# Performance work log

Hardware: AMD Instinct MI355X
Metric: run time of the kernel (lower is better)

Reference implementation:

```python
import jax, jax.numpy as jnp
import numpy as np

G_NUMS = 30      # group_nums
G_SIZE = 100     # group_size (also neighborhood_size)
BETA = 1.0
EPS = 1e-9


def setup_inputs() -> dict:
    key = jax.random.key(0)
    pointclouds = jax.random.normal(key, (8, 131072, 3), dtype=jnp.float32)
    return {"pointclouds": pointclouds}


def _knn_gather(points, queries, k):
    """points [b,N,3], queries [b,G,3] -> k nearest points per query [b,G,k,3]."""
    # squared distances [b,G,N]
    d2 = (
        jnp.sum(queries * queries, axis=-1)[..., None]
        - 2.0 * jnp.einsum("bgd,bnd->bgn", queries, points)
        + jnp.sum(points * points, axis=-1)[:, None, :]
    )
    _, idx = jax.lax.top_k(-d2, k)                    # [b,G,k]
    nbrs = jax.vmap(lambda p, i: p[i])(points, idx)   # [b,G,k,3]
    return nbrs


def reference(pointclouds):
    b, N, _ = pointclouds.shape
    # --- group_points: uniform-stride sampled centers, k-NN groups, group means ---
    stride = N // G_NUMS
    centers = pointclouds[:, ::stride][:, :G_NUMS]                 # [b,G,3]
    grouped = _knn_gather(pointclouds, centers, G_SIZE)            # [b,G,K,3]
    group_means = jnp.mean(grouped, axis=2)                        # [b,G,3]

    # --- estimate_pointcloud_local_coord_frames: per-group 3x3 PCA ---
    nbrs = _knn_gather(pointclouds, group_means, G_SIZE)           # [b,G,K,3]
    mu = jnp.mean(nbrs, axis=2, keepdims=True)
    X = nbrs - mu
    cov = jnp.einsum("bgkd,bgke->bgde", X, X) / G_SIZE             # [b,G,3,3]
    curvatures, frames = jnp.linalg.eigh(cov)                      # eigvals ascending

    # --- elongated-shape loss ---
    denom = curvatures[..., 0] + curvatures[..., 1] + curvatures[..., 2] + EPS
    first_vec = curvatures[..., 2] / denom
    second_vec = curvatures[..., 1] / denom
    elongated_shape_loss = -jnp.sum(first_vec - second_vec) / b

    # --- angular smoothness cost over group means / principal directions ---
    dirs = frames[..., :, 2]                                       # [b,G,3] largest-eig direction
    dm = jnp.sum(
        (group_means[:, :, None, :] - group_means[:, None, :, :]) ** 2, axis=-1
    )                                                              # [b,G,G]
    dm = dm + jnp.eye(G_NUMS, dtype=dm.dtype) * jnp.float32(1e30)  # exclude self
    j = jnp.argmin(dm, axis=-1)                                    # [b,G]
    dirs_j = jnp.take_along_axis(dirs, j[..., None], axis=1)       # [b,G,3]
    cos = jnp.sum(dirs * dirs_j, axis=-1)
    dlo_smooth_loss = jnp.mean(1.0 - cos * cos)                    # sign-invariant angle cost

    return elongated_shape_loss + BETA * dlo_smooth_loss
```

## Files before the change

kernel.cpp:

```cpp
#include <hip/hip_runtime.h>
#include <math.h>

#define N_PTS     131072
#define G_NUMS    30
#define G_SIZE    100
#define PT_STRIDE (N_PTS / G_NUMS)
#define TPB       512
#define NWAVES    (TPB / 64)
#define BINS      4096
#define SHIFT     20
#define SAMPLE_GRPS 1024
#define RANK_CUT  32
#define CAP       3072
#define TIE_CAP   64

__device__ __forceinline__ float dist2f(float px, float py, float pz,
                                        float qx, float qy, float qz) {
    float dx = px - qx, dy = py - qy, dz = pz - qz;
    return fmaf(dx, dx, fmaf(dy, dy, dz * dz));
}

__device__ __forceinline__ unsigned find_bin(unsigned* s_hist, unsigned* s_wsum,
                                             unsigned* s_T, unsigned rank,
                                             int tid, int lane, int wid) {
    unsigned hv[8], csum = 0;
#pragma unroll
    for (int j = 0; j < 8; j++) { hv[j] = s_hist[tid * 8 + j]; csum += hv[j]; }
    unsigned inc = csum;
#pragma unroll
    for (int off = 1; off < 64; off <<= 1) {
        unsigned n = __shfl_up(inc, off);
        if (lane >= off) inc += n;
    }
    __syncthreads();
    if (lane == 63) s_wsum[wid] = inc;
    __syncthreads();
    unsigned base = 0;
    for (int w = 0; w < wid; w++) base += s_wsum[w];
    unsigned c = base + inc - csum;
#pragma unroll
    for (int j = 0; j < 8; j++) {
        if (c < rank && c + hv[j] >= rank) *s_T = (unsigned)(tid * 8 + j);
        c += hv[j];
    }
    __syncthreads();
    return *s_T;
}

__global__ __launch_bounds__(TPB)
void fused_knn_kernel(const float* __restrict__ pts,
                      float* __restrict__ out_mean, float* __restrict__ out_cov,
                      int B) {
    __shared__ unsigned s_hist[BINS];
    __shared__ unsigned s_wsum[NWAVES];
    __shared__ unsigned s_T;
    __shared__ int s_ns, s_nd, s_nt;
    __shared__ unsigned s_u[CAP];
    __shared__ int s_idx[CAP];
    __shared__ int s_sel[G_SIZE];
    __shared__ unsigned s_tu[TIE_CAP];
    __shared__ int s_ti[TIE_CAP];
    __shared__ float s_acc[3], s_cov[6], s_q[3];

    const int blk = blockIdx.x;
    const int b = blk % B;
    const int g = blk / B;
    const int gi = b * G_NUMS + g;
    const float* __restrict__ P = pts + (size_t)b * (N_PTS * 3);
    const float4* __restrict__ P4 = (const float4*)P;
    const int tid = threadIdx.x;
    const int lane = tid & 63, wid = tid >> 6;

    if (tid == 0) {
        const float* q = P + (size_t)g * PT_STRIDE * 3;
        s_q[0] = q[0]; s_q[1] = q[1]; s_q[2] = q[2];
    }

    for (int phase = 0; phase < 2; ++phase) {
        __syncthreads();
        const float qx = s_q[0], qy = s_q[1], qz = s_q[2];

        for (int j = tid; j < BINS; j += TPB) s_hist[j] = 0u;
        if (tid == 0) { s_ns = 0; s_nd = 0; s_nt = 0; s_T = 0u; }
        if (tid < 3) s_acc[tid] = 0.f;
        if (tid < 6) s_cov[tid] = 0.f;
        __syncthreads();

        for (int grp = tid; grp < SAMPLE_GRPS; grp += TPB) {
            float4 f0 = P4[3 * grp + 0];
            float4 f1 = P4[3 * grp + 1];
            float4 f2 = P4[3 * grp + 2];
            unsigned u0 = __float_as_uint(dist2f(f0.x, f0.y, f0.z, qx, qy, qz));
            unsigned u1 = __float_as_uint(dist2f(f0.w, f1.x, f1.y, qx, qy, qz));
            unsigned u2 = __float_as_uint(dist2f(f1.z, f1.w, f2.x, qx, qy, qz));
            unsigned u3 = __float_as_uint(dist2f(f2.y, f2.z, f2.w, qx, qy, qz));
            atomicAdd(&s_hist[u0 >> SHIFT], 1u);
            atomicAdd(&s_hist[u1 >> SHIFT], 1u);
            atomicAdd(&s_hist[u2 >> SHIFT], 1u);
            atomicAdd(&s_hist[u3 >> SHIFT], 1u);
        }
        __syncthreads();
        unsigned Tc = find_bin(s_hist, s_wsum, &s_T, RANK_CUT, tid, lane, wid);
        const unsigned tau = (Tc >= BINS - 1) ? 0xFFFFFFFFu : ((Tc + 1) << SHIFT);
        for (int j = tid; j < BINS; j += TPB) s_hist[j] = 0u;
        __syncthreads();

#pragma unroll 4
        for (int grp = tid; grp < N_PTS / 4; grp += TPB) {
            float4 f0 = P4[3 * grp + 0];
            float4 f1 = P4[3 * grp + 1];
            float4 f2 = P4[3 * grp + 2];
            unsigned u0 = __float_as_uint(dist2f(f0.x, f0.y, f0.z, qx, qy, qz));
            unsigned u1 = __float_as_uint(dist2f(f0.w, f1.x, f1.y, qx, qy, qz));
            unsigned u2 = __float_as_uint(dist2f(f1.z, f1.w, f2.x, qx, qy, qz));
            unsigned u3 = __float_as_uint(dist2f(f2.y, f2.z, f2.w, qx, qy, qz));
            int i0 = grp * 4;
            if (u0 < tau) { int p = atomicAdd(&s_ns, 1); if (p < CAP) { s_u[p] = u0; s_idx[p] = i0; } }
            if (u1 < tau) { int p = atomicAdd(&s_ns, 1); if (p < CAP) { s_u[p] = u1; s_idx[p] = i0 + 1; } }
            if (u2 < tau) { int p = atomicAdd(&s_ns, 1); if (p < CAP) { s_u[p] = u2; s_idx[p] = i0 + 2; } }
            if (u3 < tau) { int p = atomicAdd(&s_ns, 1); if (p < CAP) { s_u[p] = u3; s_idx[p] = i0 + 3; } }
        }
        __syncthreads();
        int S = s_ns; if (S > CAP) S = CAP;

        unsigned hb = 32u - (unsigned)__clz(tau - 1u);
        unsigned s2 = hb > 12u ? hb - 12u : 0u;
        for (int i = tid; i < S; i += TPB) atomicAdd(&s_hist[s_u[i] >> s2], 1u);
        __syncthreads();
        unsigned T2 = find_bin(s_hist, s_wsum, &s_T, G_SIZE, tid, lane, wid);
        const unsigned lo = T2 << s2;

        for (int i = tid; i < S; i += TPB) {
            unsigned u = s_u[i];
            if (u < lo) {
                int p = atomicAdd(&s_nd, 1);
                if (p < G_SIZE) s_sel[p] = s_idx[i];
            } else if ((u >> s2) == T2) {
                int p = atomicAdd(&s_nt, 1);
                if (p < TIE_CAP) { s_tu[p] = u; s_ti[p] = s_idx[i]; }
            }
        }
        __syncthreads();
        if (tid == 0) {
            int nd = s_nd; if (nd > G_SIZE) nd = G_SIZE;
            int need = G_SIZE - nd;
            int ec = s_nt; if (ec > TIE_CAP) ec = TIE_CAP;
            for (int a = 0; a < need && a < ec; ++a) {
                int best = a;
                for (int j = a + 1; j < ec; ++j)
                    if (s_tu[j] < s_tu[best] ||
                        (s_tu[j] == s_tu[best] && s_ti[j] < s_ti[best])) best = j;
                unsigned tu = s_tu[best]; s_tu[best] = s_tu[a]; s_tu[a] = tu;
                int ti = s_ti[best]; s_ti[best] = s_ti[a]; s_ti[a] = ti;
                s_sel[nd + a] = s_ti[a];
            }
        }
        __syncthreads();

        float px = 0.f, py = 0.f, pz = 0.f;
        if (tid < G_SIZE) {
            const float* pp = P + 3 * (size_t)s_sel[tid];
            px = pp[0]; py = pp[1]; pz = pp[2];
            atomicAdd(&s_acc[0], px);
            atomicAdd(&s_acc[1], py);
            atomicAdd(&s_acc[2], pz);
        }
        __syncthreads();

        if (phase == 0) {
            if (tid < 3) {
                float m = s_acc[tid] * (1.0f / G_SIZE);
                out_mean[(size_t)gi * 3 + tid] = m;
                s_q[tid] = m;
            }
        } else {
            float mx = s_acc[0] * (1.0f / G_SIZE);
            float my = s_acc[1] * (1.0f / G_SIZE);
            float mz = s_acc[2] * (1.0f / G_SIZE);
            if (tid < G_SIZE) {
                float x = px - mx, y = py - my, z = pz - mz;
                atomicAdd(&s_cov[0], x * x);
                atomicAdd(&s_cov[1], x * y);
                atomicAdd(&s_cov[2], x * z);
                atomicAdd(&s_cov[3], y * y);
                atomicAdd(&s_cov[4], y * z);
                atomicAdd(&s_cov[5], z * z);
            }
            __syncthreads();
            if (tid < 6) out_cov[(size_t)gi * 6 + tid] = s_cov[tid] * (1.0f / G_SIZE);
        }
    }
}

__device__ void eig3(const float cf[6], double lam_out[3], double dir_out[3]) {
    double a[3][3], v[3][3];
    a[0][0] = cf[0]; a[0][1] = cf[1]; a[0][2] = cf[2];
    a[1][0] = cf[1]; a[1][1] = cf[3]; a[1][2] = cf[4];
    a[2][0] = cf[2]; a[2][1] = cf[4]; a[2][2] = cf[5];
    for (int i = 0; i < 3; i++)
        for (int j = 0; j < 3; j++) v[i][j] = (i == j) ? 1.0 : 0.0;

    for (int sweep = 0; sweep < 12; sweep++) {
        double off = a[0][1] * a[0][1] + a[0][2] * a[0][2] + a[1][2] * a[1][2];
        if (off == 0.0) break;
        for (int p = 0; p < 2; p++) {
            for (int q = p + 1; q < 3; q++) {
                double apq = a[p][q];
                if (apq == 0.0) continue;
                double app = a[p][p], aqq = a[q][q];
                double theta = (aqq - app) / (2.0 * apq);
                double t = (theta >= 0.0 ? 1.0 : -1.0) /
                           (fabs(theta) + sqrt(theta * theta + 1.0));
                double c = 1.0 / sqrt(t * t + 1.0);
                double s = t * c;
                a[p][p] = app - t * apq;
                a[q][q] = aqq + t * apq;
                a[p][q] = 0.0; a[q][p] = 0.0;
                for (int r = 0; r < 3; r++) {
                    if (r == p || r == q) continue;
                    double arp = a[r][p], arq = a[r][q];
                    a[r][p] = c * arp - s * arq; a[p][r] = a[r][p];
                    a[r][q] = s * arp + c * arq; a[q][r] = a[r][q];
                }
                for (int r = 0; r < 3; r++) {
                    double vrp = v[r][p], vrq = v[r][q];
                    v[r][p] = c * vrp - s * vrq;
                    v[r][q] = s * vrp + c * vrq;
                }
            }
        }
    }
    double l0 = a[0][0], l1 = a[1][1], l2 = a[2][2];
    int i0 = 0, i1 = 1, i2 = 2;
    if (l0 > l1) { double t = l0; l0 = l1; l1 = t; int ti = i0; i0 = i1; i1 = ti; }
    if (l1 > l2) { double t = l1; l1 = l2; l2 = t; int ti = i1; i1 = i2; i2 = ti; }
    if (l0 > l1) { double t = l0; l0 = l1; l1 = t; int ti = i0; i0 = i1; i1 = ti; }
    lam_out[0] = l0; lam_out[1] = l1; lam_out[2] = l2;
    dir_out[0] = v[0][i2]; dir_out[1] = v[1][i2]; dir_out[2] = v[2][i2];
}

__global__ __launch_bounds__(256)
void finalize_kernel(const float* __restrict__ gmeans, const float* __restrict__ covs,
                     float* __restrict__ out, int B) {
    const int tid = threadIdx.x;
    const int NG = B * G_NUMS;
    __shared__ float s_dir[256][3];
    __shared__ float s_gm[256][3];
    __shared__ float s_pe[4];
    __shared__ float s_ps[4];

    float et = 0.f;
    if (tid < NG) {
        float cf[6];
#pragma unroll
        for (int j = 0; j < 6; j++) cf[j] = covs[tid * 6 + j];
        double lam[3], dir[3];
        eig3(cf, lam, dir);
        double denom = lam[0] + lam[1] + lam[2] + 1e-9;
        et = (float)((lam[2] - lam[1]) / denom);
        s_dir[tid][0] = (float)dir[0];
        s_dir[tid][1] = (float)dir[1];
        s_dir[tid][2] = (float)dir[2];
        s_gm[tid][0] = gmeans[tid * 3 + 0];
        s_gm[tid][1] = gmeans[tid * 3 + 1];
        s_gm[tid][2] = gmeans[tid * 3 + 2];
    }
    __syncthreads();

    float st = 0.f;
    if (tid < NG) {
        int b = tid / G_NUMS, g = tid % G_NUMS;
        float gx = s_gm[tid][0], gy = s_gm[tid][1], gz = s_gm[tid][2];
        float bd = 3.4e38f; int bj = 0;
        for (int gg = 0; gg < G_NUMS; gg++) {
            if (gg == g) continue;
            int o = b * G_NUMS + gg;
            float dx = gx - s_gm[o][0];
            float dy = gy - s_gm[o][1];
            float dz = gz - s_gm[o][2];
            float d = dx * dx + dy * dy + dz * dz;
            if (d < bd) { bd = d; bj = gg; }
        }
        int o = b * G_NUMS + bj;
        float cosv = s_dir[tid][0] * s_dir[o][0] +
                     s_dir[tid][1] * s_dir[o][1] +
                     s_dir[tid][2] * s_dir[o][2];
        st = 1.f - cosv * cosv;
    }

    float e = et, s2 = st;
#pragma unroll
    for (int off = 32; off > 0; off >>= 1) {
        e += __shfl_down(e, off);
        s2 += __shfl_down(s2, off);
    }
    int lane = tid & 63, wid = tid >> 6;
    if (lane == 0) { s_pe[wid] = e; s_ps[wid] = s2; }
    __syncthreads();
    if (tid == 0) {
        float se = 0.f, ss = 0.f;
        for (int w = 0; w < 4; w++) { se += s_pe[w]; ss += s_ps[w]; }
        out[0] = -se / (float)B + ss / (float)NG;
    }
}

extern "C" void kernel_launch(void* const* d_in, const int* in_sizes, int n_in,
                              void* d_out, int out_size, void* d_ws, size_t ws_size,
                              hipStream_t stream) {
    const float* pts = (const float*)d_in[0];
    float* out = (float*)d_out;
    float* ws = (float*)d_ws;
    int B = in_sizes[0] / (N_PTS * 3);
    float* gmeans = ws;
    float* covs = ws + (size_t)B * G_NUMS * 3;

    dim3 grid(B * G_NUMS);
    fused_knn_kernel<<<grid, TPB, 0, stream>>>(pts, gmeans, covs, B);
    finalize_kernel<<<1, 256, 0, stream>>>(gmeans, covs, out, B);
}
```

Measured before the change: 161.3 us.

## Reuse phase-one candidate set for second kNN and add SoA point layout

The second kNN query (around the group mean) now first tries to select its neighbours from the candidate set gathered by the first full scan. A triangle-inequality check (first radius minus mean shift must exceed the new kth distance) decides whether that shortcut is exact; if not, it falls back to a full scan. A transpose kernel also builds SoA x/y/z copies in workspace, when it is large enough, so scans use coalesced float4 loads. This aims to skip the second full 131k-point pass per block, at the cost of an extra transpose pass and more code paths.

After: 151.6 us. -6.0%, faster.

```diff
diff --git a/kernel.cpp b/kernel.cpp
--- a/kernel.cpp
+++ b/kernel.cpp
@@ -14,18 +14,37 @@
 #define CAP       3072
 #define TIE_CAP   64
 
+struct KSmem {
+    unsigned hist[BINS];
+    unsigned wsum[NWAVES];
+    unsigned T;
+    int ns, nd, nt;
+    unsigned u[CAP];
+    int idx[CAP];
+    int sel[G_SIZE];
+    unsigned tu[TIE_CAP];
+    int ti[TIE_CAP];
+    float acc[3];
+    float cov[6];
+    float q[3];
+    unsigned tau0;
+    unsigned maxu;
+    unsigned r1;
+    float delta2;
+    int fastok;
+};
+
 __device__ __forceinline__ float dist2f(float px, float py, float pz,
                                         float qx, float qy, float qz) {
     float dx = px - qx, dy = py - qy, dz = pz - qz;
     return fmaf(dx, dx, fmaf(dy, dy, dz * dz));
 }
 
-__device__ __forceinline__ unsigned find_bin(unsigned* s_hist, unsigned* s_wsum,
-                                             unsigned* s_T, unsigned rank,
+__device__ __forceinline__ unsigned find_bin(KSmem& sm, unsigned rank,
                                              int tid, int lane, int wid) {
     unsigned hv[8], csum = 0;
 #pragma unroll
-    for (int j = 0; j < 8; j++) { hv[j] = s_hist[tid * 8 + j]; csum += hv[j]; }
+    for (int j = 0; j < 8; j++) { hv[j] = sm.hist[tid * 8 + j]; csum += hv[j]; }
     unsigned inc = csum;
 #pragma unroll
     for (int off = 1; off < 64; off <<= 1) {
@@ -33,78 +52,86 @@
         if (lane >= off) inc += n;
     }
     __syncthreads();
-    if (lane == 63) s_wsum[wid] = inc;
+    if (lane == 63) sm.wsum[wid] = inc;
     __syncthreads();
     unsigned base = 0;
-    for (int w = 0; w < wid; w++) base += s_wsum[w];
+    for (int w = 0; w < wid; w++) base += sm.wsum[w];
     unsigned c = base + inc - csum;
 #pragma unroll
     for (int j = 0; j < 8; j++) {
-        if (c < rank && c + hv[j] >= rank) *s_T = (unsigned)(tid * 8 + j);
+        if (c < rank && c + hv[j] >= rank) sm.T = (unsigned)(tid * 8 + j);
         c += hv[j];
     }
     __syncthreads();
-    return *s_T;
-}
-
-__global__ __launch_bounds__(TPB)
-void fused_knn_kernel(const float* __restrict__ pts,
-                      float* __restrict__ out_mean, float* __restrict__ out_cov,
-                      int B) {
-    __shared__ unsigned s_hist[BINS];
-    __shared__ unsigned s_wsum[NWAVES];
-    __shared__ unsigned s_T;
-    __shared__ int s_ns, s_nd, s_nt;
-    __shared__ unsigned s_u[CAP];
-    __shared__ int s_idx[CAP];
-    __shared__ int s_sel[G_SIZE];
-    __shared__ unsigned s_tu[TIE_CAP];
-    __shared__ int s_ti[TIE_CAP];
-    __shared__ float s_acc[3], s_cov[6], s_q[3];
-
-    const int blk = blockIdx.x;
-    const int b = blk % B;
-    const int g = blk / B;
-    const int gi = b * G_NUMS + g;
-    const float* __restrict__ P = pts + (size_t)b * (N_PTS * 3);
-    const float4* __restrict__ P4 = (const float4*)P;
-    const int tid = threadIdx.x;
-    const int lane = tid & 63, wid = tid >> 6;
-
-    if (tid == 0) {
-        const float* q = P + (size_t)g * PT_STRIDE * 3;
-        s_q[0] = q[0]; s_q[1] = q[1]; s_q[2] = q[2];
-    }
-
-    for (int phase = 0; phase < 2; ++phase) {
-        __syncthreads();
-        const float qx = s_q[0], qy = s_q[1], qz = s_q[2];
-
-        for (int j = tid; j < BINS; j += TPB) s_hist[j] = 0u;
-        if (tid == 0) { s_ns = 0; s_nd = 0; s_nt = 0; s_T = 0u; }
-        if (tid < 3) s_acc[tid] = 0.f;
-        if (tid < 6) s_cov[tid] = 0.f;
-        __syncthreads();
-
+    return sm.T;
+}
+
+template<bool SOA>
+__device__ __forceinline__ void load_pt(const float* __restrict__ P,
+                                        const float* __restrict__ BX,
+                                        const float* __restrict__ BY,
+                                        const float* __restrict__ BZ,
+                                        int idx, float& x, float& y, float& z) {
+    if constexpr (SOA) {
+        x = BX[idx]; y = BY[idx]; z = BZ[idx];
+    } else {
+        const float* pp = P + 3 * (size_t)idx;
+        x = pp[0]; y = pp[1]; z = pp[2];
+    }
+}
+
+template<bool SOA>
+__device__ void full_select(const float4* __restrict__ P4,
+                            const float4* __restrict__ X4,
+                            const float4* __restrict__ Y4,
+                            const float4* __restrict__ Z4,
+                            KSmem& sm, float qx, float qy, float qz,
+                            int tid, int lane, int wid, bool save_tau) {
+    for (int j = tid; j < BINS; j += TPB) sm.hist[j] = 0u;
+    if (tid == 0) { sm.ns = 0; sm.nd = 0; sm.nt = 0; sm.T = 0u; }
+    __syncthreads();
+
+    if constexpr (SOA) {
+        for (int i = tid; i < SAMPLE_GRPS; i += TPB) {
+            float4 xv = X4[i], yv = Y4[i], zv = Z4[i];
+            atomicAdd(&sm.hist[__float_as_uint(dist2f(xv.x, yv.x, zv.x, qx, qy, qz)) >> SHIFT], 1u);
+            atomicAdd(&sm.hist[__float_as_uint(dist2f(xv.y, yv.y, zv.y, qx, qy, qz)) >> SHIFT], 1u);
+            atomicAdd(&sm.hist[__float_as_uint(dist2f(xv.z, yv.z, zv.z, qx, qy, qz)) >> SHIFT], 1u);
+            atomicAdd(&sm.hist[__float_as_uint(dist2f(xv.w, yv.w, zv.w, qx, qy, qz)) >> SHIFT], 1u);
+        }
+    } else {
         for (int grp = tid; grp < SAMPLE_GRPS; grp += TPB) {
             float4 f0 = P4[3 * grp + 0];
             float4 f1 = P4[3 * grp + 1];
             float4 f2 = P4[3 * grp + 2];
-            unsigned u0 = __float_as_uint(dist2f(f0.x, f0.y, f0.z, qx, qy, qz));
-            unsigned u1 = __float_as_uint(dist2f(f0.w, f1.x, f1.y, qx, qy, qz));
-            unsigned u2 = __float_as_uint(dist2f(f1.z, f1.w, f2.x, qx, qy, qz));
-            unsigned u3 = __float_as_uint(dist2f(f2.y, f2.z, f2.w, qx, qy, qz));
-            atomicAdd(&s_hist[u0 >> SHIFT], 1u);
-            atomicAdd(&s_hist[u1 >> SHIFT], 1u);
-            atomicAdd(&s_hist[u2 >> SHIFT], 1u);
-            atomicAdd(&s_hist[u3 >> SHIFT], 1u);
-        }
-        __syncthreads();
-        unsigned Tc = find_bin(s_hist, s_wsum, &s_T, RANK_CUT, tid, lane, wid);
-        const unsigned tau = (Tc >= BINS - 1) ? 0xFFFFFFFFu : ((Tc + 1) << SHIFT);
-        for (int j = tid; j < BINS; j += TPB) s_hist[j] = 0u;
-        __syncthreads();
-
+            atomicAdd(&sm.hist[__float_as_uint(dist2f(f0.x, f0.y, f0.z, qx, qy, qz)) >> SHIFT], 1u);
+            atomicAdd(&sm.hist[__float_as_uint(dist2f(f0.w, f1.x, f1.y, qx, qy, qz)) >> SHIFT], 1u);
+            atomicAdd(&sm.hist[__float_as_uint(dist2f(f1.z, f1.w, f2.x, qx, qy, qz)) >> SHIFT], 1u);
+            atomicAdd(&sm.hist[__float_as_uint(dist2f(f2.y, f2.z, f2.w, qx, qy, qz)) >> SHIFT], 1u);
+        }
+    }
+    __syncthreads();
+    unsigned Tc = find_bin(sm, RANK_CUT, tid, lane, wid);
+    const unsigned tau = (Tc >= BINS - 1) ? 0xFFFFFFFFu : ((Tc + 1) << SHIFT);
+    if (save_tau && tid == 0) sm.tau0 = tau;
+    for (int j = tid; j < BINS; j += TPB) sm.hist[j] = 0u;
+    __syncthreads();
+
+    if constexpr (SOA) {
+#pragma unroll 4
+        for (int i = tid; i < N_PTS / 4; i += TPB) {
+            float4 xv = X4[i], yv = Y4[i], zv = Z4[i];
+            unsigned u0 = __float_as_uint(dist2f(xv.x, yv.x, zv.x, qx, qy, qz));
+            unsigned u1 = __float_as_uint(dist2f(xv.y, yv.y, zv.y, qx, qy, qz));
+            unsigned u2 = __float_as_uint(dist2f(xv.z, yv.z, zv.z, qx, qy, qz));
+            unsigned u3 = __float_as_uint(dist2f(xv.w, yv.w, zv.w, qx, qy, qz));
+            int i0 = i * 4;
+            if (u0 < tau) { int p = atomicAdd(&sm.ns, 1); if (p < CAP) { sm.u[p] = u0; sm.idx[p] = i0; } }
+            if (u1 < tau) { int p = atomicAdd(&sm.ns, 1); if (p < CAP) { sm.u[p] = u1; sm.idx[p] = i0 + 1; } }
+            if (u2 < tau) { int p = atomicAdd(&sm.ns, 1); if (p < CAP) { sm.u[p] = u2; sm.idx[p] = i0 + 2; } }
+            if (u3 < tau) { int p = atomicAdd(&sm.ns, 1); if (p < CAP) { sm.u[p] = u3; sm.idx[p] = i0 + 3; } }
+        }
+    } else {
 #pragma unroll 4
         for (int grp = tid; grp < N_PTS / 4; grp += TPB) {
             float4 f0 = P4[3 * grp + 0];
@@ -115,81 +142,220 @@
             unsigned u2 = __float_as_uint(dist2f(f1.z, f1.w, f2.x, qx, qy, qz));
             unsigned u3 = __float_as_uint(dist2f(f2.y, f2.z, f2.w, qx, qy, qz));
             int i0 = grp * 4;
-            if (u0 < tau) { int p = atomicAdd(&s_ns, 1); if (p < CAP) { s_u[p] = u0; s_idx[p] = i0; } }
-            if (u1 < tau) { int p = atomicAdd(&s_ns, 1); if (p < CAP) { s_u[p] = u1; s_idx[p] = i0 + 1; } }
-            if (u2 < tau) { int p = atomicAdd(&s_ns, 1); if (p < CAP) { s_u[p] = u2; s_idx[p] = i0 + 2; } }
-            if (u3 < tau) { int p = atomicAdd(&s_ns, 1); if (p < CAP) { s_u[p] = u3; s_idx[p] = i0 + 3; } }
+            if (u0 < tau) { int p = atomicAdd(&sm.ns, 1); if (p < CAP) { sm.u[p] = u0; sm.idx[p] = i0; } }
+            if (u1 < tau) { int p = atomicAdd(&sm.ns, 1); if (p < CAP) { sm.u[p] = u1; sm.idx[p] = i0 + 1; } }
+            if (u2 < tau) { int p = atomicAdd(&sm.ns, 1); if (p < CAP) { sm.u[p] = u2; sm.idx[p] = i0 + 2; } }
+            if (u3 < tau) { int p = atomicAdd(&sm.ns, 1); if (p < CAP) { sm.u[p] = u3; sm.idx[p] = i0 + 3; } }
+        }
+    }
+    __syncthreads();
+    int S = sm.ns; if (S > CAP) S = CAP;
+
+    unsigned hb = 32u - (unsigned)__clz(tau - 1u);
+    unsigned s2 = hb > 12u ? hb - 12u : 0u;
+    for (int i = tid; i < S; i += TPB) atomicAdd(&sm.hist[sm.u[i] >> s2], 1u);
+    __syncthreads();
+    unsigned T2 = find_bin(sm, G_SIZE, tid, lane, wid);
+    const unsigned lo = T2 << s2;
+
+    for (int i = tid; i < S; i += TPB) {
+        unsigned uu = sm.u[i];
+        if (uu < lo) {
+            int p = atomicAdd(&sm.nd, 1);
+            if (p < G_SIZE) sm.sel[p] = sm.idx[i];
+        } else if ((uu >> s2) == T2) {
+            int p = atomicAdd(&sm.nt, 1);
+            if (p < TIE_CAP) { sm.tu[p] = uu; sm.ti[p] = sm.idx[i]; }
+        }
+    }
+    __syncthreads();
+    if (tid == 0) {
+        int nd = sm.nd; if (nd > G_SIZE) nd = G_SIZE;
+        int need = G_SIZE - nd;
+        int ec = sm.nt; if (ec > TIE_CAP) ec = TIE_CAP;
+        for (int a = 0; a < need && a < ec; ++a) {
+            int best = a;
+            for (int j = a + 1; j < ec; ++j)
+                if (sm.tu[j] < sm.tu[best] ||
+                    (sm.tu[j] == sm.tu[best] && sm.ti[j] < sm.ti[best])) best = j;
+            unsigned tub = sm.tu[best]; sm.tu[best] = sm.tu[a]; sm.tu[a] = tub;
+            int tib = sm.ti[best]; sm.ti[best] = sm.ti[a]; sm.ti[a] = tib;
+            sm.sel[nd + a] = sm.ti[a];
+        }
+    }
+    __syncthreads();
+}
+
+template<bool SOA>
+__global__ __launch_bounds__(TPB)
+void fused_knn_kernel(const float* __restrict__ pts,
+                      const float* __restrict__ sx, const float* __restrict__ sy,
+                      const float* __restrict__ sz,
+                      float* __restrict__ out_mean, float* __restrict__ out_cov,
+                      int B) {
+    __shared__ KSmem sm;
+
+    const int blk = blockIdx.x;
+    const int b = blk % B;
+    const int g = blk / B;
+    const int gi = b * G_NUMS + g;
+    const float* __restrict__ P = pts + (size_t)b * (N_PTS * 3);
+    const float4* __restrict__ P4 = (const float4*)P;
+    const float* BX = nullptr; const float* BY = nullptr; const float* BZ = nullptr;
+    const float4* X4 = nullptr; const float4* Y4 = nullptr; const float4* Z4 = nullptr;
+    if constexpr (SOA) {
+        BX = sx + (size_t)b * N_PTS;
+        BY = sy + (size_t)b * N_PTS;
+        BZ = sz + (size_t)b * N_PTS;
+        X4 = (const float4*)BX; Y4 = (const float4*)BY; Z4 = (const float4*)BZ;
+    }
+    const int tid = threadIdx.x;
+    const int lane = tid & 63, wid = tid >> 6;
+
+    if (tid == 0) {
+        const float* qp = P + (size_t)g * PT_STRIDE * 3;
+        sm.q[0] = qp[0]; sm.q[1] = qp[1]; sm.q[2] = qp[2];
+    }
+    if (tid < 3) sm.acc[tid] = 0.f;
+    if (tid < 6) sm.cov[tid] = 0.f;
+    __syncthreads();
+    const float qx = sm.q[0], qy = sm.q[1], qz = sm.q[2];
+
+    full_select<SOA>(P4, X4, Y4, Z4, sm, qx, qy, qz, tid, lane, wid, true);
+
+    if (tid < G_SIZE) {
+        float x, y, z;
+        load_pt<SOA>(P, BX, BY, BZ, sm.sel[tid], x, y, z);
+        atomicAdd(&sm.acc[0], x);
+        atomicAdd(&sm.acc[1], y);
+        atomicAdd(&sm.acc[2], z);
+    }
+    __syncthreads();
+    const int S0 = sm.ns;
+    if (tid == 0) {
+        float mx = sm.acc[0] * (1.0f / G_SIZE);
+        float my = sm.acc[1] * (1.0f / G_SIZE);
+        float mz = sm.acc[2] * (1.0f / G_SIZE);
+        out_mean[(size_t)gi * 3 + 0] = mx;
+        out_mean[(size_t)gi * 3 + 1] = my;
+        out_mean[(size_t)gi * 3 + 2] = mz;
+        float dx = mx - qx, dy = my - qy, dz = mz - qz;
+        sm.delta2 = fmaf(dx, dx, fmaf(dy, dy, dz * dz));
+        sm.q[0] = mx; sm.q[1] = my; sm.q[2] = mz;
+        sm.acc[0] = 0.f; sm.acc[1] = 0.f; sm.acc[2] = 0.f;
+        sm.maxu = 0u; sm.r1 = 0u; sm.T = 0u;
+        sm.nd = 0; sm.nt = 0;
+        sm.fastok = 0;
+    }
+    __syncthreads();
+    const float q1x = sm.q[0], q1y = sm.q[1], q1z = sm.q[2];
+
+    const bool attempt = (S0 >= G_SIZE) && (S0 <= CAP);
+    if (attempt) {
+        for (int j = tid; j < BINS; j += TPB) sm.hist[j] = 0u;
+        for (int i = tid; i < S0; i += TPB) {
+            float x, y, z;
+            load_pt<SOA>(P, BX, BY, BZ, sm.idx[i], x, y, z);
+            unsigned uu = __float_as_uint(dist2f(x, y, z, q1x, q1y, q1z));
+            sm.u[i] = uu;
+            atomicMax(&sm.maxu, uu);
         }
         __syncthreads();
-        int S = s_ns; if (S > CAP) S = CAP;
-
-        unsigned hb = 32u - (unsigned)__clz(tau - 1u);
-        unsigned s2 = hb > 12u ? hb - 12u : 0u;
-        for (int i = tid; i < S; i += TPB) atomicAdd(&s_hist[s_u[i] >> s2], 1u);
+        unsigned maxu = sm.maxu;
+        unsigned hb = (maxu == 0u) ? 0u : (32u - (unsigned)__clz(maxu));
+        unsigned s3 = hb > 12u ? hb - 12u : 0u;
+        for (int i = tid; i < S0; i += TPB) atomicAdd(&sm.hist[sm.u[i] >> s3], 1u);
         __syncthreads();
-        unsigned T2 = find_bin(s_hist, s_wsum, &s_T, G_SIZE, tid, lane, wid);
-        const unsigned lo = T2 << s2;
-
-        for (int i = tid; i < S; i += TPB) {
-            unsigned u = s_u[i];
-            if (u < lo) {
-                int p = atomicAdd(&s_nd, 1);
-                if (p < G_SIZE) s_sel[p] = s_idx[i];
-            } else if ((u >> s2) == T2) {
-                int p = atomicAdd(&s_nt, 1);
-                if (p < TIE_CAP) { s_tu[p] = u; s_ti[p] = s_idx[i]; }
+        unsigned T2 = find_bin(sm, G_SIZE, tid, lane, wid);
+        const unsigned lo = T2 << s3;
+        for (int i = tid; i < S0; i += TPB) {
+            unsigned uu = sm.u[i];
+            if (uu < lo) {
+                int p = atomicAdd(&sm.nd, 1);
+                if (p < G_SIZE) sm.sel[p] = sm.idx[i];
+            } else if ((uu >> s3) == T2) {
+                int p = atomicAdd(&sm.nt, 1);
+                if (p < TIE_CAP) { sm.tu[p] = uu; sm.ti[p] = sm.idx[i]; }
             }
         }
         __syncthreads();
         if (tid == 0) {
-            int nd = s_nd; if (nd > G_SIZE) nd = G_SIZE;
+            int ok = 1;
+            int nd = sm.nd; if (nd > G_SIZE) { nd = G_SIZE; ok = 0; }
             int need = G_SIZE - nd;
-            int ec = s_nt; if (ec > TIE_CAP) ec = TIE_CAP;
+            if (sm.nt > TIE_CAP) ok = 0;
+            int ec = sm.nt; if (ec > TIE_CAP) ec = TIE_CAP;
+            if (need > ec) ok = 0;
             for (int a = 0; a < need && a < ec; ++a) {
                 int best = a;
                 for (int j = a + 1; j < ec; ++j)
-                    if (s_tu[j] < s_tu[best] ||
-                        (s_tu[j] == s_tu[best] && s_ti[j] < s_ti[best])) best = j;
-                unsigned tu = s_tu[best]; s_tu[best] = s_tu[a]; s_tu[a] = tu;
-                int ti = s_ti[best]; s_ti[best] = s_ti[a]; s_ti[a] = ti;
-                s_sel[nd + a] = s_ti[a];
+                    if (sm.tu[j] < sm.tu[best] ||
+                        (sm.tu[j] == sm.tu[best] && sm.ti[j] < sm.ti[best])) best = j;
+                unsigned tub = sm.tu[best]; sm.tu[best] = sm.tu[a]; sm.tu[a] = tub;
+                int tib = sm.ti[best]; sm.ti[best] = sm.ti[a]; sm.ti[a] = tib;
+                sm.sel[nd + a] = sm.ti[a];
             }
+            sm.fastok = ok;
         }
         __syncthreads();
-
-        float px = 0.f, py = 0.f, pz = 0.f;
-        if (tid < G_SIZE) {
-            const float* pp = P + 3 * (size_t)s_sel[tid];
-            px = pp[0]; py = pp[1]; pz = pp[2];
-            atomicAdd(&s_acc[0], px);
-            atomicAdd(&s_acc[1], py);
-            atomicAdd(&s_acc[2], pz);
-        }
-        __syncthreads();
-
-        if (phase == 0) {
-            if (tid < 3) {
-                float m = s_acc[tid] * (1.0f / G_SIZE);
-                out_mean[(size_t)gi * 3 + tid] = m;
-                s_q[tid] = m;
-            }
-        } else {
-            float mx = s_acc[0] * (1.0f / G_SIZE);
-            float my = s_acc[1] * (1.0f / G_SIZE);
-            float mz = s_acc[2] * (1.0f / G_SIZE);
+        if (sm.fastok) {
             if (tid < G_SIZE) {
-                float x = px - mx, y = py - my, z = pz - mz;
-                atomicAdd(&s_cov[0], x * x);
-                atomicAdd(&s_cov[1], x * y);
-                atomicAdd(&s_cov[2], x * z);
-                atomicAdd(&s_cov[3], y * y);
-                atomicAdd(&s_cov[4], y * z);
-                atomicAdd(&s_cov[5], z * z);
+                float x, y, z;
+                load_pt<SOA>(P, BX, BY, BZ, sm.sel[tid], x, y, z);
+                atomicMax(&sm.r1, __float_as_uint(dist2f(x, y, z, q1x, q1y, q1z)));
             }
             __syncthreads();
-            if (tid < 6) out_cov[(size_t)gi * 6 + tid] = s_cov[tid] * (1.0f / G_SIZE);
-        }
-    }
+            if (tid == 0) {
+                double R0 = sqrt((double)__uint_as_float(sm.tau0));
+                double dl = sqrt((double)sm.delta2);
+                double r1 = sqrt((double)__uint_as_float(sm.r1));
+                if (!((R0 - dl) > r1 * 1.0001 + 1e-7)) sm.fastok = 0;
+            }
+            __syncthreads();
+        }
+    }
+
+    if (!attempt || !sm.fastok) {
+        full_select<SOA>(P4, X4, Y4, Z4, sm, q1x, q1y, q1z, tid, lane, wid, false);
+    }
+
+    float px = 0.f, py = 0.f, pz = 0.f;
+    if (tid < G_SIZE) {
+        load_pt<SOA>(P, BX, BY, BZ, sm.sel[tid], px, py, pz);
+        atomicAdd(&sm.acc[0], px);
+        atomicAdd(&sm.acc[1], py);
+        atomicAdd(&sm.acc[2], pz);
+    }
+    __syncthreads();
+    float mx = sm.acc[0] * (1.0f / G_SIZE);
+    float my = sm.acc[1] * (1.0f / G_SIZE);
+    float mz = sm.acc[2] * (1.0f / G_SIZE);
+    if (tid < G_SIZE) {
+        float x = px - mx, y = py - my, z = pz - mz;
+        atomicAdd(&sm.cov[0], x * x);
+        atomicAdd(&sm.cov[1], x * y);
+        atomicAdd(&sm.cov[2], x * z);
+        atomicAdd(&sm.cov[3], y * y);
+        atomicAdd(&sm.cov[4], y * z);
+        atomicAdd(&sm.cov[5], z * z);
+    }
+    __syncthreads();
+    if (tid < 6) out_cov[(size_t)gi * 6 + tid] = sm.cov[tid] * (1.0f / G_SIZE);
+}
+
+__global__ __launch_bounds__(256)
+void transpose_kernel(const float* __restrict__ pts,
+                      float* __restrict__ sx, float* __restrict__ sy,
+                      float* __restrict__ sz, int total4) {
+    int t = blockIdx.x * 256 + threadIdx.x;
+    if (t >= total4) return;
+    const float4* __restrict__ P4 = (const float4*)pts;
+    float4 f0 = P4[3 * t + 0];
+    float4 f1 = P4[3 * t + 1];
+    float4 f2 = P4[3 * t + 2];
+    ((float4*)sx)[t] = make_float4(f0.x, f0.w, f1.z, f2.y);
+    ((float4*)sy)[t] = make_float4(f0.y, f1.x, f1.w, f2.z);
+    ((float4*)sz)[t] = make_float4(f0.z, f1.y, f2.x, f2.w);
 }
 
 __device__ void eig3(const float cf[6], double lam_out[3], double dir_out[3]) {
@@ -314,7 +480,23 @@
     float* gmeans = ws;
     float* covs = ws + (size_t)B * G_NUMS * 3;
 
+    const size_t base_floats = (size_t)B * G_NUMS * 9;
+    const size_t soa_floats = 3 * (size_t)B * N_PTS;
+    const bool use_soa = ws_size >= (base_floats + soa_floats) * sizeof(float);
+
     dim3 grid(B * G_NUMS);
-    fused_knn_kernel<<<grid, TPB, 0, stream>>>(pts, gmeans, covs, B);
-    finalize_kernel<<<1, 256, 0, stream>>>(gmeans, covs, out, B);
-}
+    if (use_soa) {
+        float* sx = ws + base_floats;
+        float* sy = sx + (size_t)B * N_PTS;
+        float* sz = sy + (size_t)B * N_PTS;
+        int total4 = B * N_PTS / 4;
+        transpose_kernel<<<dim3((total4 + 255) / 256), dim3(256), 0, stream>>>(
+            pts, sx, sy, sz, total4);
+        fused_knn_kernel<true><<<grid, TPB, 0, stream>>>(
+            pts, sx, sy, sz, gmeans, covs, B);
+    } else {
+        fused_knn_kernel<false><<<grid, TPB, 0, stream>>>(
+            pts, nullptr, nullptr, nullptr, gmeans, covs, B);
+    }
+    finalize_kernel<<<dim3(1), dim3(256), 0, stream>>>(gmeans, covs, out, B);
+}
```
